# Kernel optimization log

Hardware: AMD Instinct MI355X
Metric: run time of the kernel (lower is better)

The kernel has to match this reference:

```python
import math
import jax, jax.numpy as jnp
import numpy as np

L, H, W_SIZE, EPS = 4, 4, 64, 1e-5


def _sinusoidal_pe(T, D):
    pos = np.arange(T, dtype=np.float32)[:, None]
    div = np.exp(np.arange(0, D, 2, dtype=np.float32) * -(math.log(10000.0) / D))
    pe = np.zeros((T, D), dtype=np.float32)
    pe[:, 0::2] = np.sin(pos * div)
    pe[:, 1::2] = np.cos(pos * div)
    return jnp.asarray(pe)


def _layernorm(x, g, b):
    mu = jnp.mean(x, axis=-1, keepdims=True)
    var = jnp.mean(jnp.square(x - mu), axis=-1, keepdims=True)
    return (x - mu) * jax.lax.rsqrt(var + EPS) * g + b


def setup_inputs() -> dict:
    key = jax.random.key(0)
    B, T, D, F = 4, 2048, 256, 1024
    ks = jax.random.split(key, 8)
    s = 0.02
    return {
        "tokens": jax.random.normal(ks[0], (B, T, D), jnp.float32),
        "Wqkv": jax.random.normal(ks[1], (L, 3 * D, D), jnp.float32) * s,
        "bqkv": jnp.zeros((L, 3 * D), jnp.float32),
        "Wo": jax.random.normal(ks[2], (L, D, D), jnp.float32) * s,
        "bo": jnp.zeros((L, D), jnp.float32),
        "W1": jax.random.normal(ks[3], (L, F, D), jnp.float32) * s,
        "b1": jnp.zeros((L, F), jnp.float32),
        "W2": jax.random.normal(ks[4], (L, D, F), jnp.float32) * s,
        "b2": jnp.zeros((L, D), jnp.float32),
        "ln1_g": jnp.ones((L, D), jnp.float32),
        "ln1_b": jnp.zeros((L, D), jnp.float32),
        "ln2_g": jnp.ones((L, D), jnp.float32),
        "ln2_b": jnp.zeros((L, D), jnp.float32),
        "lnf_g": jnp.ones((D,), jnp.float32),
        "lnf_b": jnp.zeros((D,), jnp.float32),
    }


def reference(tokens, Wqkv, bqkv, Wo, bo, W1, b1, W2, b2,
              ln1_g, ln1_b, ln2_g, ln2_b, lnf_g, lnf_b):
    B, T, D = tokens.shape
    hd = D // H
    x = tokens + _sinusoidal_pe(T, D)[None]  # (B,T,D)

    # sliding-window causal mask: i attends to max(0, i-W+1)..i
    idx = jnp.arange(T)
    i, j = idx[:, None], idx[None, :]
    allowed = (j <= i) & (j >= i - W_SIZE + 1)
    bias = jnp.where(allowed, 0.0, -1e9).astype(jnp.float32)  # (T,T)

    def step(x, p):
        Wqkv, bqkv, Wo, bo, W1, b1, W2, b2, g1, be1, g2, be2 = p
        x2 = _layernorm(x, g1, be1)
        qkv = x2 @ Wqkv.T + bqkv                      # (B,T,3D)
        q, k, v = jnp.split(qkv, 3, axis=-1)
        q = q.reshape(B, T, H, hd)
        k = k.reshape(B, T, H, hd)
        v = v.reshape(B, T, H, hd)
        scores = jnp.einsum("bthd,bshd->bhts", q, k) / math.sqrt(hd)
        attn = jax.nn.softmax(scores + bias, axis=-1)
        o = jnp.einsum("bhts,bshd->bthd", attn, v).reshape(B, T, D)
        x = x + o @ Wo.T + bo
        x3 = _layernorm(x, g2, be2)
        h = jax.nn.gelu(x3 @ W1.T + b1, approximate=False)
        x = x + h @ W2.T + b2
        return x, None

    x, _ = jax.lax.scan(step, x, (Wqkv, bqkv, Wo, bo, W1, b1, W2, b2,
                                  ln1_g, ln1_b, ln2_g, ln2_b))
    return _layernorm(x, lnf_g, lnf_b)
```

## Files before the change

### kernel.cpp

```cpp
#include <hip/hip_runtime.h>
#include <hip/hip_bf16.h>
#include <math.h>

#define BB 4
#define TT 2048
#define DD 256
#define FF 1024
#define NL 4

typedef __bf16 bf16x8 __attribute__((ext_vector_type(8)));
typedef float f32x4 __attribute__((ext_vector_type(4)));

__global__ __launch_bounds__(256) void f2b_all_kernel(const float4* __restrict__ wq,
                                                      const float4* __restrict__ wo,
                                                      const float4* __restrict__ w1,
                                                      const float4* __restrict__ w2,
                                                      ushort4* __restrict__ dst) {
  int gi = blockIdx.x * 256 + threadIdx.x;
  const float4* src;
  int off;
  if (gi < 196608)      { src = wq; off = gi; }
  else if (gi < 262144) { src = wo; off = gi - 196608; }
  else if (gi < 524288) { src = w1; off = gi - 262144; }
  else                  { src = w2; off = gi - 524288; }
  float4 v = src[off];
  ushort4 o;
  o.x = __hip_bfloat16_raw(__float2bfloat16(v.x)).x;
  o.y = __hip_bfloat16_raw(__float2bfloat16(v.y)).x;
  o.z = __hip_bfloat16_raw(__float2bfloat16(v.z)).x;
  o.w = __hip_bfloat16_raw(__float2bfloat16(v.w)).x;
  dst[gi] = o;
}

__global__ __launch_bounds__(256) void pe_ln_kernel(const float* __restrict__ tokens,
                                                    const float* __restrict__ g,
                                                    const float* __restrict__ b,
                                                    float* __restrict__ x,
                                                    __hip_bfloat16* __restrict__ sb) {
  int row = blockIdx.x * 4 + (threadIdx.x >> 6);
  int lane = threadIdx.x & 63;
  int t = row & (TT - 1);
  const float* xr = tokens + (size_t)row * DD;
  float v[4];
  float s = 0.f;
#pragma unroll
  for (int i = 0; i < 4; ++i) {
    int d = lane + 64 * i;
    int i2 = d & ~1;
    float freq = expf((float)i2 * -(9.210340371976184f / 256.f));
    float ang = (float)t * freq;
    float pe = (d & 1) ? cosf(ang) : sinf(ang);
    v[i] = xr[d] + pe;
    s += v[i];
  }
#pragma unroll
  for (int off = 32; off; off >>= 1) s += __shfl_xor(s, off, 64);
  float mu = s * (1.f / DD);
  float vs = 0.f;
#pragma unroll
  for (int i = 0; i < 4; ++i) { float dd = v[i] - mu; vs = fmaf(dd, dd, vs); }
#pragma unroll
  for (int off = 32; off; off >>= 1) vs += __shfl_xor(vs, off, 64);
  float rr = rsqrtf(vs * (1.f / DD) + 1e-5f);
#pragma unroll
  for (int i = 0; i < 4; ++i) {
    int d = lane + 64 * i;
    x[(size_t)row * DD + d] = v[i];
    sb[(size_t)row * DD + d] = __float2bfloat16((v[i] - mu) * rr * g[d] + b[d]);
  }
}

template <int MW, int NW, int ACT>
__global__ __launch_bounds__(256) void mgemm_kernel(
    const __hip_bfloat16* __restrict__ A, const __hip_bfloat16* __restrict__ B,
    const float* __restrict__ bias, __hip_bfloat16* __restrict__ Cout,
    int M, int N, int K) {
  constexpr int BM = 32 * MW, BN = 32 * NW;
  constexpr int ROWS = BM + BN;
  constexpr int NINST = ROWS / 16;
  __shared__ __align__(16) __hip_bfloat16 sm[ROWS * 32];
  const int tid = threadIdx.x;
  const int wave = tid >> 6, lane = tid & 63;
  const int m0 = blockIdx.y * BM, n0 = blockIdx.x * BN;
  const int wm = (wave >> 1) * (16 * MW), wn = (wave & 1) * (16 * NW);
  const int qk = lane >> 4;
  const int lr = lane & 15;
  const int srow = lane >> 2;
  const int scol = (lane & 3) * 8;

  f32x4 acc[MW][NW] = {};

  for (int kt = 0; kt < K; kt += 32) {
    __syncthreads();
#pragma unroll
    for (int i = 0; i < (NINST + 3) / 4; ++i) {
      int inst = i * 4 + wave;
      if (inst < NINST) {
        int r = inst * 16 + srow;
        const __hip_bfloat16* g =
            (r < BM) ? (A + (size_t)(m0 + r) * K + kt + scol)
                     : (B + (size_t)(n0 + (r - BM)) * K + kt + scol);
        __builtin_amdgcn_global_load_lds(
            (const __attribute__((address_space(1))) unsigned int*)g,
            (__attribute__((address_space(3))) unsigned int*)(sm + inst * 512),
            16, 0, 0);
      }
    }
    __syncthreads();
    bf16x8 af[MW], bfr[NW];
#pragma unroll
    for (int mi = 0; mi < MW; ++mi)
      af[mi] = *(const bf16x8*)(sm + (wm + mi * 16 + lr) * 32 + qk * 8);
#pragma unroll
    for (int ni = 0; ni < NW; ++ni)
      bfr[ni] = *(const bf16x8*)(sm + (BM + wn + ni * 16 + lr) * 32 + qk * 8);
#pragma unroll
    for (int mi = 0; mi < MW; ++mi)
#pragma unroll
      for (int ni = 0; ni < NW; ++ni)
        acc[mi][ni] = __builtin_amdgcn_mfma_f32_16x16x32_bf16(
            af[mi], bfr[ni], acc[mi][ni], 0, 0, 0);
  }

#pragma unroll
  for (int mi = 0; mi < MW; ++mi) {
#pragma unroll
    for (int ni = 0; ni < NW; ++ni) {
      int col = n0 + wn + ni * 16 + lr;
      float bv = bias[col];
#pragma unroll
      for (int r = 0; r < 4; ++r) {
        int row = m0 + wm + mi * 16 + qk * 4 + r;
        float v = acc[mi][ni][r] + bv;
        if (ACT == 1) v = 0.5f * v * (1.f + erff(v * 0.70710678118654752f));
        Cout[(size_t)row * N + col] = __float2bfloat16(v);
      }
    }
  }
}

template <int FIN>
__global__ __launch_bounds__(256) void mgemm_ln_kernel(
    const __hip_bfloat16* __restrict__ A, const __hip_bfloat16* __restrict__ B,
    const float* __restrict__ bias, const float* __restrict__ res,
    const float* __restrict__ g, const float* __restrict__ bb,
    float* __restrict__ xout, void* __restrict__ yout, int K) {
  constexpr int NINST = 17;
  __shared__ __align__(16) __hip_bfloat16 sm[(16 + 256) * 32];
  __shared__ float red1[4][16], red2[4][16];
  const int tid = threadIdx.x;
  const int wave = tid >> 6, lane = tid & 63;
  const int quad = lane >> 4, lr = lane & 15;
  const int m0 = blockIdx.x * 16;
  const int srow = lane >> 2, scol = (lane & 3) * 8;

  f32x4 acc[4] = {};

  for (int kt = 0; kt < K; kt += 32) {
    __syncthreads();
#pragma unroll
    for (int i = 0; i < 5; ++i) {
      int inst = i * 4 + wave;
      if (inst < NINST) {
        int r = inst * 16 + srow;
        const __hip_bfloat16* gp =
            (r < 16) ? (A + (size_t)(m0 + r) * K + kt + scol)
                     : (B + (size_t)(r - 16) * K + kt + scol);
        __builtin_amdgcn_global_load_lds(
            (const __attribute__((address_space(1))) unsigned int*)gp,
            (__attribute__((address_space(3))) unsigned int*)(sm + inst * 512),
            16, 0, 0);
      }
    }
    __syncthreads();
    bf16x8 af = *(const bf16x8*)(sm + lr * 32 + quad * 8);
    bf16x8 bfr[4];
#pragma unroll
    for (int ni = 0; ni < 4; ++ni)
      bfr[ni] = *(const bf16x8*)(sm + (16 + wave * 64 + ni * 16 + lr) * 32 + quad * 8);
#pragma unroll
    for (int ni = 0; ni < 4; ++ni)
      acc[ni] = __builtin_amdgcn_mfma_f32_16x16x32_bf16(af, bfr[ni], acc[ni], 0, 0, 0);
  }

  float v[4][4];
  float s1[4] = {}, s2[4] = {};
#pragma unroll
  for (int ni = 0; ni < 4; ++ni) {
    int col = wave * 64 + ni * 16 + lr;
    float bv = bias[col];
#pragma unroll
    for (int r = 0; r < 4; ++r) {
      int row = m0 + quad * 4 + r;
      float val = acc[ni][r] + bv + res[(size_t)row * DD + col];
      v[ni][r] = val;
      s1[r] += val;
      s2[r] = fmaf(val, val, s2[r]);
    }
  }
#pragma unroll
  for (int r = 0; r < 4; ++r) {
#pragma unroll
    for (int off = 8; off; off >>= 1) {
      s1[r] += __shfl_xor(s1[r], off, 64);
      s2[r] += __shfl_xor(s2[r], off, 64);
    }
  }
  if (lr == 0) {
#pragma unroll
    for (int r = 0; r < 4; ++r) {
      red1[wave][quad * 4 + r] = s1[r];
      red2[wave][quad * 4 + r] = s2[r];
    }
  }
  __syncthreads();
#pragma unroll
  for (int r = 0; r < 4; ++r) {
    int rl = quad * 4 + r;
    float ssum = red1[0][rl] + red1[1][rl] + red1[2][rl] + red1[3][rl];
    float qsum = red2[0][rl] + red2[1][rl] + red2[2][rl] + red2[3][rl];
    float mu = ssum * (1.f / DD);
    float var = qsum * (1.f / DD) - mu * mu;
    float rr = rsqrtf(var + 1e-5f);
    int row = m0 + rl;
#pragma unroll
    for (int ni = 0; ni < 4; ++ni) {
      int col = wave * 64 + ni * 16 + lr;
      float y = (v[ni][r] - mu) * rr * g[col] + bb[col];
      if (FIN) {
        ((float*)yout)[(size_t)row * DD + col] = y;
      } else {
        ((__hip_bfloat16*)yout)[(size_t)row * DD + col] = __float2bfloat16(y);
        xout[(size_t)row * DD + col] = v[ni][r];
      }
    }
  }
}

__global__ __launch_bounds__(256) void attn_kernel(const __hip_bfloat16* __restrict__ qkv,
                                                   __hip_bfloat16* __restrict__ o) {
  __shared__ __align__(16) __hip_bfloat16 Ks[128][72];
  __shared__ __align__(16) __hip_bfloat16 Vt[64 * 136];
  __shared__ __align__(16) __hip_bfloat16 Ps[4][16][136];
  const int bh = blockIdx.y;
  const int b = bh >> 2, h = bh & 3;
  const int t0 = blockIdx.x * 64;
  const int sbase = t0 - 63;
  const int tid = threadIdx.x;

  const __hip_bfloat16* kb = qkv + (size_t)(b * TT) * 768 + 256 + h * 64;
  const __hip_bfloat16* vb = kb + 256;
  union U8 { uint4 u; __hip_bfloat16 hx[8]; };
#pragma unroll
  for (int it = 0; it < 4; ++it) {
    int f = tid + it * 256;
    int si = f >> 3;
    int c8 = f & 7;
    int s = sbase + si;
    U8 kr, vr;
    kr.u = make_uint4(0, 0, 0, 0); vr.u = make_uint4(0, 0, 0, 0);
    if (s >= 0 && s < TT) {
      kr.u = *(const uint4*)&kb[(size_t)s * 768 + 8 * c8];
      vr.u = *(const uint4*)&vb[(size_t)s * 768 + 8 * c8];
    }
    *(uint4*)&Ks[si][c8 * 8] = kr.u;
    int pc = (si >> 3) ^ c8;
#pragma unroll
    for (int j = 0; j < 8; ++j) Vt[(c8 * 8 + j) * 136 + pc * 8 + (si & 7)] = vr.hx[j];
  }
  __syncthreads();

  const int wave = tid >> 6, lane = tid & 63;
  const int quad = lane >> 4, lr = lane & 15;

  const __hip_bfloat16* qrow = qkv + (size_t)(b * TT + t0 + wave * 16 + lr) * 768 + h * 64;
  bf16x8 qa0 = *(const bf16x8*)(qrow + quad * 8);
  bf16x8 qa1 = *(const bf16x8*)(qrow + 32 + quad * 8);
  f32x4 sc[8];
#pragma unroll
  for (int c = 0; c < 8; ++c) {
    f32x4 a = {};
    bf16x8 kf0 = *(const bf16x8*)&Ks[c * 16 + lr][quad * 8];
    a = __builtin_amdgcn_mfma_f32_16x16x32_bf16(qa0, kf0, a, 0, 0, 0);
    bf16x8 kf1 = *(const bf16x8*)&Ks[c * 16 + lr][32 + quad * 8];
    a = __builtin_amdgcn_mfma_f32_16x16x32_bf16(qa1, kf1, a, 0, 0, 0);
    sc[c] = a;
  }

#pragma unroll
  for (int reg = 0; reg < 4; ++reg) {
    int dt = wave * 16 + quad * 4 + reg;
    float pv[8];
    float mx = -1e30f;
#pragma unroll
    for (int c = 0; c < 8; ++c) {
      int si = c * 16 + lr;
      float v = sc[c][reg] * 0.125f;
      bool ok = (si >= dt) && (si <= dt + 63) && (sbase + si >= 0);
      v = ok ? v : -1e30f;
      pv[c] = v;
      mx = fmaxf(mx, v);
    }
#pragma unroll
    for (int off = 8; off; off >>= 1) mx = fmaxf(mx, __shfl_xor(mx, off, 64));
    float l = 0.f;
#pragma unroll
    for (int c = 0; c < 8; ++c) { float e = __expf(pv[c] - mx); pv[c] = e; l += e; }
#pragma unroll
    for (int off = 8; off; off >>= 1) l += __shfl_xor(l, off, 64);
    float rinv = 1.f / l;
#pragma unroll
    for (int c = 0; c < 8; ++c)
      Ps[wave][quad * 4 + reg][c * 16 + lr] = __float2bfloat16(pv[c] * rinv);
  }

  __hip_bfloat16* obase = o + (size_t)(b * TT) * DD + h * 64;
#pragma unroll
  for (int ct = 0; ct < 4; ++ct) {
    f32x4 acc = {};
#pragma unroll
    for (int kk = 0; kk < 4; ++kk) {
      bf16x8 pa = *(const bf16x8*)&Ps[wave][lr][kk * 32 + quad * 8];
      int dd = ct * 16 + lr;
      bf16x8 vf = *(const bf16x8*)&Vt[dd * 136 + (((kk * 4 + quad) ^ (dd >> 3)) * 8)];
      acc = __builtin_amdgcn_mfma_f32_16x16x32_bf16(pa, vf, acc, 0, 0, 0);
    }
#pragma unroll
    for (int reg = 0; reg < 4; ++reg) {
      int t = t0 + wave * 16 + quad * 4 + reg;
      obase[(size_t)t * DD + ct * 16 + lr] = __float2bfloat16(acc[reg]);
    }
  }
}

extern "C" void kernel_launch(void* const* d_in, const int* in_sizes, int n_in,
                              void* d_out, int out_size, void* d_ws, size_t ws_size,
                              hipStream_t stream) {
  const float* tokens = (const float*)d_in[0];
  const float* Wqkv = (const float*)d_in[1];
  const float* bqkv = (const float*)d_in[2];
  const float* Wo   = (const float*)d_in[3];
  const float* bo   = (const float*)d_in[4];
  const float* W1   = (const float*)d_in[5];
  const float* b1   = (const float*)d_in[6];
  const float* W2   = (const float*)d_in[7];
  const float* b2   = (const float*)d_in[8];
  const float* ln1g = (const float*)d_in[9];
  const float* ln1b = (const float*)d_in[10];
  const float* ln2g = (const float*)d_in[11];
  const float* ln2b = (const float*)d_in[12];
  const float* lnfg = (const float*)d_in[13];
  const float* lnfb = (const float*)d_in[14];
  float* out = (float*)d_out;

  const int M = BB * TT;
  const int ND = M * DD;

  float* x = (float*)d_ws;
  __hip_bfloat16* sb  = (__hip_bfloat16*)(x + ND);
  __hip_bfloat16* big = sb + (size_t)M * DD;
  __hip_bfloat16* wqb = big + (size_t)M * FF;
  __hip_bfloat16* wob = wqb + (size_t)NL * 3 * DD * DD;
  __hip_bfloat16* w1b = wob + (size_t)NL * DD * DD;
  __hip_bfloat16* w2b = w1b + (size_t)NL * FF * DD;

  f2b_all_kernel<<<3072, 256, 0, stream>>>(
      (const float4*)Wqkv, (const float4*)Wo, (const float4*)W1,
      (const float4*)W2, (ushort4*)wqb);

  pe_ln_kernel<<<M / 4, 256, 0, stream>>>(tokens, ln1g, ln1b, x, sb);

  for (int l = 0; l < NL; ++l) {
    mgemm_kernel<4, 3, 0><<<dim3(768 / 96, M / 128), 256, 0, stream>>>(
        sb, wqb + (size_t)l * 768 * DD, bqkv + l * 768, big, M, 768, DD);
    attn_kernel<<<dim3(TT / 64, BB * 4), 256, 0, stream>>>(big, sb);
    mgemm_ln_kernel<0><<<M / 16, 256, 0, stream>>>(
        sb, wob + (size_t)l * DD * DD, bo + l * DD, x,
        ln2g + l * DD, ln2b + l * DD, x, sb, DD);
    mgemm_kernel<4, 4, 1><<<dim3(FF / 128, M / 128), 256, 0, stream>>>(
        sb, w1b + (size_t)l * FF * DD, b1 + l * FF, big, M, FF, DD);
    if (l < NL - 1) {
      mgemm_ln_kernel<0><<<M / 16, 256, 0, stream>>>(
          big, w2b + (size_t)l * DD * FF, b2 + l * DD, x,
          ln1g + (l + 1) * DD, ln1b + (l + 1) * DD, x, sb, FF);
    } else {
      mgemm_ln_kernel<1><<<M / 16, 256, 0, stream>>>(
          big, w2b + (size_t)l * DD * FF, b2 + l * DD, x,
          lnfg, lnfb, nullptr, out, FF);
    }
  }
}
```

Measured before the change: 388.9 us.

## Double row tile in fused GEMM+LayerNorm and merge prologue kernels

The fused GEMM+residual+LayerNorm kernel now handles 32 rows per block instead of 16. Each wave does two MFMA row-fragments against the same B fragments, so each weight tile loaded into shared memory is reused across twice as many rows and half as many blocks launch. The weight bf16 conversion and the positional-encoding LayerNorm kernels are merged into one launch, which removes one kernel launch. In exchange the block uses more shared memory and registers, and the grid has fewer blocks, which may lower occupancy and load balance.

```diff
diff --git a/kernel.cpp b/kernel.cpp
--- a/kernel.cpp
+++ b/kernel.cpp
@@ -11,33 +11,31 @@
 typedef __bf16 bf16x8 __attribute__((ext_vector_type(8)));
 typedef float f32x4 __attribute__((ext_vector_type(4)));
 
-__global__ __launch_bounds__(256) void f2b_all_kernel(const float4* __restrict__ wq,
-                                                      const float4* __restrict__ wo,
-                                                      const float4* __restrict__ w1,
-                                                      const float4* __restrict__ w2,
-                                                      ushort4* __restrict__ dst) {
-  int gi = blockIdx.x * 256 + threadIdx.x;
-  const float4* src;
-  int off;
-  if (gi < 196608)      { src = wq; off = gi; }
-  else if (gi < 262144) { src = wo; off = gi - 196608; }
-  else if (gi < 524288) { src = w1; off = gi - 262144; }
-  else                  { src = w2; off = gi - 524288; }
-  float4 v = src[off];
-  ushort4 o;
-  o.x = __hip_bfloat16_raw(__float2bfloat16(v.x)).x;
-  o.y = __hip_bfloat16_raw(__float2bfloat16(v.y)).x;
-  o.z = __hip_bfloat16_raw(__float2bfloat16(v.z)).x;
-  o.w = __hip_bfloat16_raw(__float2bfloat16(v.w)).x;
-  dst[gi] = o;
-}
-
-__global__ __launch_bounds__(256) void pe_ln_kernel(const float* __restrict__ tokens,
-                                                    const float* __restrict__ g,
-                                                    const float* __restrict__ b,
-                                                    float* __restrict__ x,
-                                                    __hip_bfloat16* __restrict__ sb) {
-  int row = blockIdx.x * 4 + (threadIdx.x >> 6);
+__global__ __launch_bounds__(256) void prologue_kernel(
+    const float4* __restrict__ wq, const float4* __restrict__ wo,
+    const float4* __restrict__ w1, const float4* __restrict__ w2,
+    ushort4* __restrict__ dst,
+    const float* __restrict__ tokens, const float* __restrict__ g,
+    const float* __restrict__ b, float* __restrict__ x,
+    __hip_bfloat16* __restrict__ sb) {
+  if (blockIdx.x < 3072) {
+    int gi = blockIdx.x * 256 + threadIdx.x;
+    const float4* src;
+    int off;
+    if (gi < 196608)      { src = wq; off = gi; }
+    else if (gi < 262144) { src = wo; off = gi - 196608; }
+    else if (gi < 524288) { src = w1; off = gi - 262144; }
+    else                  { src = w2; off = gi - 524288; }
+    float4 v = src[off];
+    ushort4 o;
+    o.x = __hip_bfloat16_raw(__float2bfloat16(v.x)).x;
+    o.y = __hip_bfloat16_raw(__float2bfloat16(v.y)).x;
+    o.z = __hip_bfloat16_raw(__float2bfloat16(v.z)).x;
+    o.w = __hip_bfloat16_raw(__float2bfloat16(v.w)).x;
+    dst[gi] = o;
+    return;
+  }
+  int row = (blockIdx.x - 3072) * 4 + (threadIdx.x >> 6);
   int lane = threadIdx.x & 63;
   int t = row & (TT - 1);
   const float* xr = tokens + (size_t)row * DD;
@@ -145,16 +143,17 @@
     const float* __restrict__ bias, const float* __restrict__ res,
     const float* __restrict__ g, const float* __restrict__ bb,
     float* __restrict__ xout, void* __restrict__ yout, int K) {
-  constexpr int NINST = 17;
-  __shared__ __align__(16) __hip_bfloat16 sm[(16 + 256) * 32];
-  __shared__ float red1[4][16], red2[4][16];
+  constexpr int BM = 32;
+  constexpr int NINST = (BM + 256) / 16;
+  __shared__ __align__(16) __hip_bfloat16 sm[(BM + 256) * 32];
+  __shared__ float red1[4][BM], red2[4][BM];
   const int tid = threadIdx.x;
   const int wave = tid >> 6, lane = tid & 63;
   const int quad = lane >> 4, lr = lane & 15;
-  const int m0 = blockIdx.x * 16;
+  const int m0 = blockIdx.x * BM;
   const int srow = lane >> 2, scol = (lane & 3) * 8;
 
-  f32x4 acc[4] = {};
+  f32x4 acc[2][4] = {};
 
   for (int kt = 0; kt < K; kt += 32) {
     __syncthreads();
@@ -164,8 +163,8 @@
       if (inst < NINST) {
         int r = inst * 16 + srow;
         const __hip_bfloat16* gp =
-            (r < 16) ? (A + (size_t)(m0 + r) * K + kt + scol)
-                     : (B + (size_t)(r - 16) * K + kt + scol);
+            (r < BM) ? (A + (size_t)(m0 + r) * K + kt + scol)
+                     : (B + (size_t)(r - BM) * K + kt + scol);
         __builtin_amdgcn_global_load_lds(
             (const __attribute__((address_space(1))) unsigned int*)gp,
             (__attribute__((address_space(3))) unsigned int*)(sm + inst * 512),
@@ -173,68 +172,81 @@
       }
     }
     __syncthreads();
-    bf16x8 af = *(const bf16x8*)(sm + lr * 32 + quad * 8);
-    bf16x8 bfr[4];
+    bf16x8 af[2], bfr[4];
+#pragma unroll
+    for (int mi = 0; mi < 2; ++mi)
+      af[mi] = *(const bf16x8*)(sm + (mi * 16 + lr) * 32 + quad * 8);
 #pragma unroll
     for (int ni = 0; ni < 4; ++ni)
-      bfr[ni] = *(const bf16x8*)(sm + (16 + wave * 64 + ni * 16 + lr) * 32 + quad * 8);
-#pragma unroll
-    for (int ni = 0; ni < 4; ++ni)
-      acc[ni] = __builtin_amdgcn_mfma_f32_16x16x32_bf16(af, bfr[ni], acc[ni], 0, 0, 0);
-  }
-
-  float v[4][4];
-  float s1[4] = {}, s2[4] = {};
-#pragma unroll
-  for (int ni = 0; ni < 4; ++ni) {
-    int col = wave * 64 + ni * 16 + lr;
-    float bv = bias[col];
-#pragma unroll
-    for (int r = 0; r < 4; ++r) {
-      int row = m0 + quad * 4 + r;
-      float val = acc[ni][r] + bv + res[(size_t)row * DD + col];
-      v[ni][r] = val;
-      s1[r] += val;
-      s2[r] = fmaf(val, val, s2[r]);
-    }
-  }
-#pragma unroll
-  for (int r = 0; r < 4; ++r) {
-#pragma unroll
-    for (int off = 8; off; off >>= 1) {
-      s1[r] += __shfl_xor(s1[r], off, 64);
-      s2[r] += __shfl_xor(s2[r], off, 64);
-    }
-  }
-  if (lr == 0) {
-#pragma unroll
-    for (int r = 0; r < 4; ++r) {
-      red1[wave][quad * 4 + r] = s1[r];
-      red2[wave][quad * 4 + r] = s2[r];
-    }
-  }
-  __syncthreads();
-#pragma unroll
-  for (int r = 0; r < 4; ++r) {
-    int rl = quad * 4 + r;
-    float ssum = red1[0][rl] + red1[1][rl] + red1[2][rl] + red1[3][rl];
-    float qsum = red2[0][rl] + red2[1][rl] + red2[2][rl] + red2[3][rl];
-    float mu = ssum * (1.f / DD);
-    float var = qsum * (1.f / DD) - mu * mu;
-    float rr = rsqrtf(var + 1e-5f);
-    int row = m0 + rl;
+      bfr[ni] = *(const bf16x8*)(sm + (BM + wave * 64 + ni * 16 + lr) * 32 + quad * 8);
+#pragma unroll
+    for (int mi = 0; mi < 2; ++mi)
+#pragma unroll
+      for (int ni = 0; ni < 4; ++ni)
+        acc[mi][ni] = __builtin_amdgcn_mfma_f32_16x16x32_bf16(
+            af[mi], bfr[ni], acc[mi][ni], 0, 0, 0);
+  }
+
+  float v[2][4][4];
+  float s1[2][4] = {}, s2[2][4] = {};
+#pragma unroll
+  for (int mi = 0; mi < 2; ++mi)
 #pragma unroll
     for (int ni = 0; ni < 4; ++ni) {
       int col = wave * 64 + ni * 16 + lr;
-      float y = (v[ni][r] - mu) * rr * g[col] + bb[col];
-      if (FIN) {
-        ((float*)yout)[(size_t)row * DD + col] = y;
-      } else {
-        ((__hip_bfloat16*)yout)[(size_t)row * DD + col] = __float2bfloat16(y);
-        xout[(size_t)row * DD + col] = v[ni][r];
-      }
-    }
-  }
+      float bv = bias[col];
+#pragma unroll
+      for (int r = 0; r < 4; ++r) {
+        int row = m0 + mi * 16 + quad * 4 + r;
+        float val = acc[mi][ni][r] + bv + res[(size_t)row * DD + col];
+        v[mi][ni][r] = val;
+        s1[mi][r] += val;
+        s2[mi][r] = fmaf(val, val, s2[mi][r]);
+      }
+    }
+#pragma unroll
+  for (int mi = 0; mi < 2; ++mi)
+#pragma unroll
+    for (int r = 0; r < 4; ++r) {
+#pragma unroll
+      for (int off = 8; off; off >>= 1) {
+        s1[mi][r] += __shfl_xor(s1[mi][r], off, 64);
+        s2[mi][r] += __shfl_xor(s2[mi][r], off, 64);
+      }
+    }
+  if (lr == 0) {
+#pragma unroll
+    for (int mi = 0; mi < 2; ++mi)
+#pragma unroll
+      for (int r = 0; r < 4; ++r) {
+        red1[wave][mi * 16 + quad * 4 + r] = s1[mi][r];
+        red2[wave][mi * 16 + quad * 4 + r] = s2[mi][r];
+      }
+  }
+  __syncthreads();
+#pragma unroll
+  for (int mi = 0; mi < 2; ++mi)
+#pragma unroll
+    for (int r = 0; r < 4; ++r) {
+      int rl = mi * 16 + quad * 4 + r;
+      float ssum = red1[0][rl] + red1[1][rl] + red1[2][rl] + red1[3][rl];
+      float qsum = red2[0][rl] + red2[1][rl] + red2[2][rl] + red2[3][rl];
+      float mu = ssum * (1.f / DD);
+      float var = qsum * (1.f / DD) - mu * mu;
+      float rr = rsqrtf(var + 1e-5f);
+      int row = m0 + rl;
+#pragma unroll
+      for (int ni = 0; ni < 4; ++ni) {
+        int col = wave * 64 + ni * 16 + lr;
+        float y = (v[mi][ni][r] - mu) * rr * g[col] + bb[col];
+        if (FIN) {
+          ((float*)yout)[(size_t)row * DD + col] = y;
+        } else {
+          ((__hip_bfloat16*)yout)[(size_t)row * DD + col] = __float2bfloat16(y);
+          xout[(size_t)row * DD + col] = v[mi][ni][r];
+        }
+      }
+    }
 }
 
 __global__ __launch_bounds__(256) void attn_kernel(const __hip_bfloat16* __restrict__ qkv,
@@ -364,27 +376,25 @@
   __hip_bfloat16* w1b = wob + (size_t)NL * DD * DD;
   __hip_bfloat16* w2b = w1b + (size_t)NL * FF * DD;
 
-  f2b_all_kernel<<<3072, 256, 0, stream>>>(
+  prologue_kernel<<<3072 + M / 4, 256, 0, stream>>>(
       (const float4*)Wqkv, (const float4*)Wo, (const float4*)W1,
-      (const float4*)W2, (ushort4*)wqb);
-
-  pe_ln_kernel<<<M / 4, 256, 0, stream>>>(tokens, ln1g, ln1b, x, sb);
+      (const float4*)W2, (ushort4*)wqb, tokens, ln1g, ln1b, x, sb);
 
   for (int l = 0; l < NL; ++l) {
     mgemm_kernel<4, 3, 0><<<dim3(768 / 96, M / 128), 256, 0, stream>>>(
         sb, wqb + (size_t)l * 768 * DD, bqkv + l * 768, big, M, 768, DD);
     attn_kernel<<<dim3(TT / 64, BB * 4), 256, 0, stream>>>(big, sb);
-    mgemm_ln_kernel<0><<<M / 16, 256, 0, stream>>>(
+    mgemm_ln_kernel<0><<<M / 32, 256, 0, stream>>>(
         sb, wob + (size_t)l * DD * DD, bo + l * DD, x,
         ln2g + l * DD, ln2b + l * DD, x, sb, DD);
     mgemm_kernel<4, 4, 1><<<dim3(FF / 128, M / 128), 256, 0, stream>>>(
         sb, w1b + (size_t)l * FF * DD, b1 + l * FF, big, M, FF, DD);
     if (l < NL - 1) {
-      mgemm_ln_kernel<0><<<M / 16, 256, 0, stream>>>(
+      mgemm_ln_kernel<0><<<M / 32, 256, 0, stream>>>(
           big, w2b + (size_t)l * DD * FF, b2 + l * DD, x,
           ln1g + (l + 1) * DD, ln1b + (l + 1) * DD, x, sb, FF);
     } else {
-      mgemm_ln_kernel<1><<<M / 16, 256, 0, stream>>>(
+      mgemm_ln_kernel<1><<<M / 32, 256, 0, stream>>>(
           big, w2b + (size_t)l * DD * FF, b2 + l * DD, x,
           lnfg, lnfb, nullptr, out, FF);
     }
```

Result: no change. 389.2 us (+0.1%).
